# Optimization experiments

Hardware: AMD Instinct MI355X
Metric: run time of the kernel (lower is better)

## Reference

```python
import jax, jax.numpy as jnp
import numpy as np

D = 64  # query_dimensions (power of 2, required by Hadamard)
N, L, H = 8, 8192, 8


def fwht(x):
    """Unnormalized fast Walsh-Hadamard transform along the last axis.
    x: (..., d), d a power of 2."""
    orig_shape = x.shape
    d = orig_shape[-1]
    x = x.reshape(-1, d)
    h = 1
    while h < d:  # log2(d) stages, static under jit
        x = x.reshape(-1, d // (2 * h), 2, h)
        a, b = x[:, :, 0, :], x[:, :, 1, :]
        x = jnp.stack([a + b, a - b], axis=2).reshape(-1, d)
        h *= 2
    return x.reshape(orig_shape)


def setup_inputs() -> dict:
    key = jax.random.key(0)
    kx, kb, kg, ks, kp = jax.random.split(key, 5)
    x = jax.random.normal(kx, (N, L, H, D), dtype=jnp.float32)
    # B: random signs in {-1, +1}
    B = jnp.where(jax.random.bernoulli(kb, 0.5, (D,)), 1.0, -1.0).astype(jnp.float32)
    # G: standard normal
    G = jax.random.normal(kg, (D,), dtype=jnp.float32)
    # S: chi(df=D) samples, divided by ||G|| (as in new_feature_map)
    chi_samples = jnp.linalg.norm(jax.random.normal(ks, (D, D), dtype=jnp.float32), axis=1)
    S = chi_samples / jnp.linalg.norm(G)
    # P: random permutation of [0, D)
    P = jax.random.permutation(kp, D).astype(jnp.int32)
    return {"x": x, "B": B, "G": G, "S": S, "P": P}


def reference(x, B, G, S, P):
    # softmax_temp defaults to 1/sqrt(query_dimensions)
    softmax_temp = 1.0 / np.sqrt(D)
    x_shape = x.shape
    y = (x * np.sqrt(softmax_temp)).reshape(-1, D)
    y = fwht(y * B)          # H B x
    y = y[:, P] * G          # G P H B x
    y = fwht(y) * S          # S H G P H B x
    return (np.sqrt(1.0 / D) * y).reshape(x_shape)
```

## Files before the change

kernel.cpp:

```cpp
#include <hip/hip_runtime.h>


typedef float f32x4 __attribute__((ext_vector_type(4)));
typedef unsigned u32x2 __attribute__((ext_vector_type(2)));

__device__ __forceinline__ float partner32(float v, bool hh) {
    const unsigned u = __float_as_uint(v);
    const u32x2 r = __builtin_amdgcn_permlane32_swap(u, u, false, false);
    return __uint_as_float(hh ? r.x : r.y);
}

#define FSTAGE32(H)                                                 \
    _Pragma("unroll")                                               \
    for (int i = 0; i < 32; i += 2*(H)) {                           \
        _Pragma("unroll")                                           \
        for (int j = 0; j < (H); ++j) {                             \
            const float a = y[i+j], b = y[i+j+(H)];                 \
            y[i+j] = a + b; y[i+j+(H)] = a - b;                     \
        }                                                           \
    }

__global__ __launch_bounds__(128) void fastfood_kernel(
    const float* __restrict__ x,
    const float* __restrict__ Bv,
    const float* __restrict__ Gv,
    const float* __restrict__ Sv,
    const int*   __restrict__ Pv,
    float* __restrict__ out,
    int ntiles)
{
    __shared__ float lds_all[2 * 2048];
    const int l  = threadIdx.x & 63;
    const int wv = threadIdx.x >> 6;
    float* lds = &lds_all[wv * 2048];

    const int wid    = blockIdx.x * 2 + wv;
    const int nwaves = gridDim.x * 2;

    const int hi = l >> 4;
    const int lo = l & 15;
    const int e0 = lo << 2;
    const int rr = l & 31;
    const bool hh = (l >= 32);
    const int cb = hh ? 32 : 0;
    const int swzr = (rr & 15) << 2;

    const float c1 = 0.35355339059327373f;
    const float c2 = 0.125f;

    const float bs0 = Bv[e0+0]*c1, bs1 = Bv[e0+1]*c1, bs2 = Bv[e0+2]*c1, bs3 = Bv[e0+3]*c1;
    const float gg0 = Gv[e0+0],    gg1 = Gv[e0+1],    gg2 = Gv[e0+2],    gg3 = Gv[e0+3];
    const float ss0 = Sv[e0+0]*c2, ss1 = Sv[e0+1]*c2, ss2 = Sv[e0+2]*c2, ss3 = Sv[e0+3]*c2;
    const int   p0  = Pv[e0+0],    p1  = Pv[e0+1],    p2  = Pv[e0+2],    p3  = Pv[e0+3];

    const f32x4* __restrict__ xin  = (const f32x4*)x;
    f32x4* __restrict__       yout = (f32x4*)out;

    int t = wid;
    if (t >= ntiles) return;

    f32x4 st[8];
    {
        const long long tb = (long long)t * 512;
        #pragma unroll
        for (int c = 0; c < 8; ++c) st[c] = xin[tb + c*64 + l];
    }

    for (; t < ntiles; t += nwaves) {
        const long long tb = (long long)t * 512;

        #pragma unroll
        for (int c = 0; c < 8; ++c) {
            const int r = 4*c + hi;
            f32x4 v = st[c];
            v.x *= bs0; v.y *= bs1; v.z *= bs2; v.w *= bs3;
            *(f32x4*)&lds[r*64 + (e0 ^ ((r & 15) << 2))] = v;
        }

        float y[32];
        #pragma unroll
        for (int k = 0; k < 8; ++k) {
            const f32x4 v = *(const f32x4*)&lds[rr*64 + ((cb + 4*k) ^ swzr)];
            y[4*k+0] = v.x; y[4*k+1] = v.y; y[4*k+2] = v.z; y[4*k+3] = v.w;
        }

        FSTAGE32(1) FSTAGE32(2) FSTAGE32(4) FSTAGE32(8) FSTAGE32(16)
        #pragma unroll
        for (int i = 0; i < 32; ++i) {
            const float opp = partner32(y[i], hh);
            y[i] = hh ? (opp - y[i]) : (y[i] + opp);
        }

        #pragma unroll
        for (int k = 0; k < 8; ++k) {
            f32x4 v;
            v.x = y[4*k+0]; v.y = y[4*k+1]; v.z = y[4*k+2]; v.w = y[4*k+3];
            *(f32x4*)&lds[rr*64 + ((cb + 4*k) ^ swzr)] = v;
        }

        #pragma unroll
        for (int c = 0; c < 8; ++c) {
            const int r  = 4*c + hi;
            const int rb = r * 64;
            const int sw = (r & 15) << 2;
            const float a0 = lds[rb + (p0 ^ sw)];
            const float a1 = lds[rb + (p1 ^ sw)];
            const float a2 = lds[rb + (p2 ^ sw)];
            const float a3 = lds[rb + (p3 ^ sw)];
            f32x4 v;
            v.x = a0 * gg0; v.y = a1 * gg1; v.z = a2 * gg2; v.w = a3 * gg3;
            *(f32x4*)&lds[rb + (e0 ^ sw)] = v;
        }

        if (t + nwaves < ntiles) {
            const long long nb = (long long)(t + nwaves) * 512;
            #pragma unroll
            for (int c = 0; c < 8; ++c) st[c] = xin[nb + c*64 + l];
        }

        #pragma unroll
        for (int k = 0; k < 8; ++k) {
            const f32x4 v = *(const f32x4*)&lds[rr*64 + ((cb + 4*k) ^ swzr)];
            y[4*k+0] = v.x; y[4*k+1] = v.y; y[4*k+2] = v.z; y[4*k+3] = v.w;
        }

        FSTAGE32(1) FSTAGE32(2) FSTAGE32(4) FSTAGE32(8) FSTAGE32(16)
        #pragma unroll
        for (int i = 0; i < 32; ++i) {
            const float opp = partner32(y[i], hh);
            y[i] = hh ? (opp - y[i]) : (y[i] + opp);
        }

        #pragma unroll
        for (int k = 0; k < 8; ++k) {
            f32x4 v;
            v.x = y[4*k+0]; v.y = y[4*k+1]; v.z = y[4*k+2]; v.w = y[4*k+3];
            *(f32x4*)&lds[rr*64 + ((cb + 4*k) ^ swzr)] = v;
        }

        #pragma unroll
        for (int c = 0; c < 8; ++c) {
            const int r = 4*c + hi;
            f32x4 v = *(const f32x4*)&lds[r*64 + (e0 ^ ((r & 15) << 2))];
            v.x *= ss0; v.y *= ss1; v.z *= ss2; v.w *= ss3;
            __builtin_nontemporal_store(v, &yout[tb + c*64 + l]);
        }
    }
}

extern "C" void kernel_launch(void* const* d_in, const int* in_sizes, int n_in,
                              void* d_out, int out_size, void* d_ws, size_t ws_size,
                              hipStream_t stream) {
    const float* x = (const float*)d_in[0];
    const float* B = (const float*)d_in[1];
    const float* G = (const float*)d_in[2];
    const float* S = (const float*)d_in[3];
    const int*   P = (const int*)d_in[4];
    float* out = (float*)d_out;

    const int ntiles = in_sizes[0] / 2048;

    const int block = 128;
    const int grid  = 2048;
    fastfood_kernel<<<grid, block, 0, stream>>>(x, B, G, S, P, out, ntiles);
}
```

Baseline: 47.45 us.

## Halve per-wave tile to 16 rows with two-level cross-lane butterfly

Each wave now handles 16 rows instead of 32 per tile. Each lane keeps 16 values, does 4 in-register butterfly stages, then two cross-lane stages using permlane16_swap and permlane32_swap. The grid is doubled, LDS and prefetch registers are halved, and the permutation indices are packed into one register. The aim is lower register and LDS pressure and higher occupancy, at the cost of an extra cross-lane stage per transform and more waves.

```diff
diff --git a/kernel.cpp b/kernel.cpp
--- a/kernel.cpp
+++ b/kernel.cpp
@@ -4,15 +4,26 @@
 typedef float f32x4 __attribute__((ext_vector_type(4)));
 typedef unsigned u32x2 __attribute__((ext_vector_type(2)));
 
-__device__ __forceinline__ float partner32(float v, bool hh) {
+__device__ __forceinline__ float partner32(float v, bool hb) {
     const unsigned u = __float_as_uint(v);
     const u32x2 r = __builtin_amdgcn_permlane32_swap(u, u, false, false);
-    return __uint_as_float(hh ? r.x : r.y);
+    return __uint_as_float(hb ? r.x : r.y);
 }
 
-#define FSTAGE32(H)                                                 \
+__device__ __forceinline__ float partner16(float v, bool hb, int l) {
+#if __has_builtin(__builtin_amdgcn_permlane16_swap)
+    const unsigned u = __float_as_uint(v);
+    const u32x2 r = __builtin_amdgcn_permlane16_swap(u, u, false, false);
+    return __uint_as_float(hb ? r.x : r.y);
+#else
+    (void)hb; (void)l;
+    return __shfl_xor(v, 16);
+#endif
+}
+
+#define FSTAGE16(H)                                                 \
     _Pragma("unroll")                                               \
-    for (int i = 0; i < 32; i += 2*(H)) {                           \
+    for (int i = 0; i < 16; i += 2*(H)) {                           \
         _Pragma("unroll")                                           \
         for (int j = 0; j < (H); ++j) {                             \
             const float a = y[i+j], b = y[i+j+(H)];                 \
@@ -29,10 +40,10 @@
     float* __restrict__ out,
     int ntiles)
 {
-    __shared__ float lds_all[2 * 2048];
+    __shared__ float lds_all[2 * 1024];
     const int l  = threadIdx.x & 63;
     const int wv = threadIdx.x >> 6;
-    float* lds = &lds_all[wv * 2048];
+    float* lds = &lds_all[wv * 1024];
 
     const int wid    = blockIdx.x * 2 + wv;
     const int nwaves = gridDim.x * 2;
@@ -40,10 +51,11 @@
     const int hi = l >> 4;
     const int lo = l & 15;
     const int e0 = lo << 2;
-    const int rr = l & 31;
-    const bool hh = (l >= 32);
-    const int cb = hh ? 32 : 0;
-    const int swzr = (rr & 15) << 2;
+    const int rr = l & 15;
+    const int cq = hi << 4;
+    const int swzr = rr << 2;
+    const bool h16 = (l & 16) != 0;
+    const bool h32 = (l & 32) != 0;
 
     const float c1 = 0.35355339059327373f;
     const float c2 = 0.125f;
@@ -51,7 +63,8 @@
     const float bs0 = Bv[e0+0]*c1, bs1 = Bv[e0+1]*c1, bs2 = Bv[e0+2]*c1, bs3 = Bv[e0+3]*c1;
     const float gg0 = Gv[e0+0],    gg1 = Gv[e0+1],    gg2 = Gv[e0+2],    gg3 = Gv[e0+3];
     const float ss0 = Sv[e0+0]*c2, ss1 = Sv[e0+1]*c2, ss2 = Sv[e0+2]*c2, ss3 = Sv[e0+3]*c2;
-    const int   p0  = Pv[e0+0],    p1  = Pv[e0+1],    p2  = Pv[e0+2],    p3  = Pv[e0+3];
+    const unsigned pp = (unsigned)Pv[e0+0] | ((unsigned)Pv[e0+1] << 8)
+                      | ((unsigned)Pv[e0+2] << 16) | ((unsigned)Pv[e0+3] << 24);
 
     const f32x4* __restrict__ xin  = (const f32x4*)x;
     f32x4* __restrict__       yout = (f32x4*)out;
@@ -59,89 +72,99 @@
     int t = wid;
     if (t >= ntiles) return;
 
-    f32x4 st[8];
+    f32x4 st[4];
     {
-        const long long tb = (long long)t * 512;
+        const long long tb = (long long)t * 256;
         #pragma unroll
-        for (int c = 0; c < 8; ++c) st[c] = xin[tb + c*64 + l];
+        for (int c = 0; c < 4; ++c) st[c] = xin[tb + c*64 + l];
     }
 
     for (; t < ntiles; t += nwaves) {
-        const long long tb = (long long)t * 512;
+        const long long tb = (long long)t * 256;
 
         #pragma unroll
-        for (int c = 0; c < 8; ++c) {
+        for (int c = 0; c < 4; ++c) {
             const int r = 4*c + hi;
             f32x4 v = st[c];
             v.x *= bs0; v.y *= bs1; v.z *= bs2; v.w *= bs3;
-            *(f32x4*)&lds[r*64 + (e0 ^ ((r & 15) << 2))] = v;
+            *(f32x4*)&lds[r*64 + (e0 ^ (r << 2))] = v;
         }
 
-        float y[32];
+        float y[16];
         #pragma unroll
-        for (int k = 0; k < 8; ++k) {
-            const f32x4 v = *(const f32x4*)&lds[rr*64 + ((cb + 4*k) ^ swzr)];
+        for (int k = 0; k < 4; ++k) {
+            const f32x4 v = *(const f32x4*)&lds[rr*64 + ((cq + 4*k) ^ swzr)];
             y[4*k+0] = v.x; y[4*k+1] = v.y; y[4*k+2] = v.z; y[4*k+3] = v.w;
         }
 
-        FSTAGE32(1) FSTAGE32(2) FSTAGE32(4) FSTAGE32(8) FSTAGE32(16)
+        FSTAGE16(1) FSTAGE16(2) FSTAGE16(4) FSTAGE16(8)
         #pragma unroll
-        for (int i = 0; i < 32; ++i) {
-            const float opp = partner32(y[i], hh);
-            y[i] = hh ? (opp - y[i]) : (y[i] + opp);
+        for (int i = 0; i < 16; ++i) {
+            const float opp = partner16(y[i], h16, l);
+            y[i] = h16 ? (opp - y[i]) : (y[i] + opp);
+        }
+        #pragma unroll
+        for (int i = 0; i < 16; ++i) {
+            const float opp = partner32(y[i], h32);
+            y[i] = h32 ? (opp - y[i]) : (y[i] + opp);
         }
 
         #pragma unroll
-        for (int k = 0; k < 8; ++k) {
+        for (int k = 0; k < 4; ++k) {
             f32x4 v;
             v.x = y[4*k+0]; v.y = y[4*k+1]; v.z = y[4*k+2]; v.w = y[4*k+3];
-            *(f32x4*)&lds[rr*64 + ((cb + 4*k) ^ swzr)] = v;
+            *(f32x4*)&lds[rr*64 + ((cq + 4*k) ^ swzr)] = v;
         }
 
         #pragma unroll
-        for (int c = 0; c < 8; ++c) {
+        for (int c = 0; c < 4; ++c) {
             const int r  = 4*c + hi;
             const int rb = r * 64;
-            const int sw = (r & 15) << 2;
-            const float a0 = lds[rb + (p0 ^ sw)];
-            const float a1 = lds[rb + (p1 ^ sw)];
-            const float a2 = lds[rb + (p2 ^ sw)];
-            const float a3 = lds[rb + (p3 ^ sw)];
+            const int sw = r << 2;
+            const float a0 = lds[rb + (((pp      ) & 63u) ^ sw)];
+            const float a1 = lds[rb + (((pp >>  8) & 63u) ^ sw)];
+            const float a2 = lds[rb + (((pp >> 16) & 63u) ^ sw)];
+            const float a3 = lds[rb + (((pp >> 24) & 63u) ^ sw)];
             f32x4 v;
             v.x = a0 * gg0; v.y = a1 * gg1; v.z = a2 * gg2; v.w = a3 * gg3;
             *(f32x4*)&lds[rb + (e0 ^ sw)] = v;
         }
 
         if (t + nwaves < ntiles) {
-            const long long nb = (long long)(t + nwaves) * 512;
+            const long long nb = (long long)(t + nwaves) * 256;
             #pragma unroll
-            for (int c = 0; c < 8; ++c) st[c] = xin[nb + c*64 + l];
+            for (int c = 0; c < 4; ++c) st[c] = xin[nb + c*64 + l];
         }
 
         #pragma unroll
-        for (int k = 0; k < 8; ++k) {
-            const f32x4 v = *(const f32x4*)&lds[rr*64 + ((cb + 4*k) ^ swzr)];
+        for (int k = 0; k < 4; ++k) {
+            const f32x4 v = *(const f32x4*)&lds[rr*64 + ((cq + 4*k) ^ swzr)];
             y[4*k+0] = v.x; y[4*k+1] = v.y; y[4*k+2] = v.z; y[4*k+3] = v.w;
         }
 
-        FSTAGE32(1) FSTAGE32(2) FSTAGE32(4) FSTAGE32(8) FSTAGE32(16)
+        FSTAGE16(1) FSTAGE16(2) FSTAGE16(4) FSTAGE16(8)
         #pragma unroll
-        for (int i = 0; i < 32; ++i) {
-            const float opp = partner32(y[i], hh);
-            y[i] = hh ? (opp - y[i]) : (y[i] + opp);
+        for (int i = 0; i < 16; ++i) {
+            const float opp = partner16(y[i], h16, l);
+            y[i] = h16 ? (opp - y[i]) : (y[i] + opp);
+        }
+        #pragma unroll
+        for (int i = 0; i < 16; ++i) {
+            const float opp = partner32(y[i], h32);
+            y[i] = h32 ? (opp - y[i]) : (y[i] + opp);
         }
 
         #pragma unroll
-        for (int k = 0; k < 8; ++k) {
+        for (int k = 0; k < 4; ++k) {
             f32x4 v;
             v.x = y[4*k+0]; v.y = y[4*k+1]; v.z = y[4*k+2]; v.w = y[4*k+3];
-            *(f32x4*)&lds[rr*64 + ((cb + 4*k) ^ swzr)] = v;
+            *(f32x4*)&lds[rr*64 + ((cq + 4*k) ^ swzr)] = v;
         }
 
         #pragma unroll
-        for (int c = 0; c < 8; ++c) {
+        for (int c = 0; c < 4; ++c) {
             const int r = 4*c + hi;
-            f32x4 v = *(const f32x4*)&lds[r*64 + (e0 ^ ((r & 15) << 2))];
+            f32x4 v = *(const f32x4*)&lds[r*64 + (e0 ^ (r << 2))];
             v.x *= ss0; v.y *= ss1; v.z *= ss2; v.w *= ss3;
             __builtin_nontemporal_store(v, &yout[tb + c*64 + l]);
         }
@@ -158,9 +181,9 @@
     const int*   P = (const int*)d_in[4];
     float* out = (float*)d_out;
 
-    const int ntiles = in_sizes[0] / 2048;
+    const int ntiles = in_sizes[0] / 1024;
 
     const int block = 128;
-    const int grid  = 2048;
+    const int grid  = 4096;
     fastfood_kernel<<<grid, block, 0, stream>>>(x, B, G, S, P, out, ntiles);
 }
```

Result: no change. 47.03 us (-0.9%).
